# Kernel tuning notes

Hardware: AMD Instinct MI355X
Metric: run time of the kernel (lower is better)

Reference implementation:

```python
import itertools
import jax, jax.numpy as jnp
import numpy as np

NDIMS = 3
SPATIAL = (160, 160, 160)


def affine_to_dense_shift(matrix, shape, shift_center=True):
    # matrix: [ndims, ndims+1] -> displacement field [*shape, ndims]
    dt = matrix.dtype
    grids = jnp.meshgrid(*[jnp.arange(s, dtype=dt) for s in shape], indexing='ij')
    mesh = jnp.stack(grids, axis=-1)  # [D,H,W,3]
    if shift_center:
        mesh = mesh - (jnp.asarray(shape, dt) - 1.0) / 2.0
    ones = jnp.ones(mesh.shape[:-1] + (1,), dt)
    homog = jnp.concatenate([mesh, ones], axis=-1)  # [D,H,W,4]
    loc = jnp.einsum('dhwj,ij->dhwi', homog, matrix)  # [D,H,W,3]
    return loc - mesh  # displacement, invariant to the center shift


def interpn_linear(vol, loc):
    # vol: [D,H,W,C], loc: [D,H,W,3] absolute voxel coords. fill_value=None -> clip.
    D, H, W = vol.shape[:NDIMS]
    max_loc = jnp.asarray([D - 1, H - 1, W - 1], loc.dtype)
    loc = jnp.clip(loc, 0.0, max_loc)
    loc0 = jnp.clip(jnp.floor(loc), 0.0, max_loc)
    loc1 = jnp.clip(loc0 + 1.0, 0.0, max_loc)
    w_lo = loc1 - loc          # weight of the lower corner (voxelmorph convention)
    w_hi = 1.0 - w_lo          # weight of the upper corner
    loc0i = loc0.astype(jnp.int32)
    loc1i = loc1.astype(jnp.int32)
    vol_flat = vol.reshape(-1, vol.shape[-1])  # [D*H*W, C]
    out = jnp.zeros(loc.shape[:-1] + (vol.shape[-1],), vol.dtype)
    for corner in itertools.product([0, 1], repeat=NDIMS):  # 8 trilinear corners
        ii = (loc1i if corner[0] else loc0i)[..., 0]
        jj = (loc1i if corner[1] else loc0i)[..., 1]
        kk = (loc1i if corner[2] else loc0i)[..., 2]
        flat = (ii * H + jj) * W + kk
        vals = jnp.take(vol_flat, flat.reshape(-1), axis=0).reshape(out.shape)
        wt = jnp.ones(loc.shape[:-1], loc.dtype)
        for d, b in enumerate(corner):
            wt = wt * (w_hi[..., d] if b else w_lo[..., d])
        out = out + vals * wt[..., None]
    return out


def _single_transform(vol_b, aff_b):
    shift = affine_to_dense_shift(aff_b, SPATIAL, shift_center=True)  # [D,H,W,3]
    grids = jnp.meshgrid(*[jnp.arange(s, dtype=shift.dtype) for s in SPATIAL], indexing='ij')
    grid = jnp.stack(grids, axis=-1)
    return interpn_linear(vol_b, grid + shift)


def setup_inputs() -> dict:
    key = jax.random.key(0)
    k1, k2 = jax.random.split(key)
    vol = jax.random.normal(k1, (4, *SPATIAL, 2), dtype=jnp.float32)
    # near-identity affine so most sampled coordinates stay in-bounds
    eye = jnp.broadcast_to(jnp.eye(NDIMS, NDIMS + 1, dtype=jnp.float32), (4, NDIMS, NDIMS + 1))
    trf = eye + 0.1 * jax.random.normal(k2, (4, NDIMS, NDIMS + 1), dtype=jnp.float32)
    return {"vol": vol, "trf": trf}


def reference(vol, trf):
    return jax.vmap(_single_transform)(vol, trf)
```

## Files before the change

### kernel.cpp

```cpp
#include <hip/hip_runtime.h>


constexpr int D = 160, H = 160, W = 160, C = 2;
constexpr unsigned VOX_PER_B = D * H * W;
constexpr int TI = 4, TJ = 8, TK = 32;
constexpr unsigned NTI = D / TI;
constexpr unsigned NTJ = H / TJ;
constexpr unsigned NTK = W / TK;
constexpr unsigned TPV = NTI * NTJ * NTK;
constexpr unsigned NBLOCKS = 4u * TPV;
constexpr unsigned NXCD = 8;
constexpr unsigned CHUNK = NBLOCKS / NXCD;

struct VPair { float2 lo, hi; };

struct Gset { int p00, p01, p10, p11; float wxl, wyl, wzl; };

__device__ __forceinline__ Gset mkset(float lx, float ly, float lz)
{
    const float mx = 159.0f;
    lx = fminf(fmaxf(lx, 0.0f), mx);
    ly = fminf(fmaxf(ly, 0.0f), mx);
    lz = fminf(fmaxf(lz, 0.0f), mx);

    float fx0 = floorf(lx), fy0 = floorf(ly), fz0 = floorf(lz);
    float fx1 = fminf(fx0 + 1.0f, mx);
    float fy1 = fminf(fy0 + 1.0f, mx);
    float fz1 = fminf(fz0 + 1.0f, mx);

    int ix0 = (int)fx0, iy0 = (int)fy0, iz0 = (int)fz0;
    int ix1 = (int)fx1, iy1 = (int)fy1;

    Gset g;
    g.wxl = fx1 - lx; g.wyl = fy1 - ly; g.wzl = fz1 - lz;

    int zb = min(iz0, W - 2);
    int r0 = ix0 * H, r1 = ix1 * H;
    g.p00 = (r0 + iy0) * W + zb;
    g.p01 = (r0 + iy1) * W + zb;
    g.p10 = (r1 + iy0) * W + zb;
    g.p11 = (r1 + iy1) * W + zb;
    return g;
}

__device__ __forceinline__ float2 interp(VPair q00, VPair q01, VPair q10, VPair q11,
                                         const Gset& g)
{
    float wzl = g.wzl, wzh = 1.0f - wzl;
    float wyl = g.wyl, wyh = 1.0f - wyl;
    float wxl = g.wxl, wxh = 1.0f - wxl;

    float zx00 = q00.lo.x * wzl + q00.hi.x * wzh, zy00 = q00.lo.y * wzl + q00.hi.y * wzh;
    float zx01 = q01.lo.x * wzl + q01.hi.x * wzh, zy01 = q01.lo.y * wzl + q01.hi.y * wzh;
    float zx10 = q10.lo.x * wzl + q10.hi.x * wzh, zy10 = q10.lo.y * wzl + q10.hi.y * wzh;
    float zx11 = q11.lo.x * wzl + q11.hi.x * wzh, zy11 = q11.lo.y * wzl + q11.hi.y * wzh;

    float yx0 = zx00 * wyl + zx01 * wyh, yy0 = zy00 * wyl + zy01 * wyh;
    float yx1 = zx10 * wyl + zx11 * wyh, yy1 = zy10 * wyl + zy11 * wyh;

    float2 o;
    o.x = yx0 * wxl + yx1 * wxh;
    o.y = yy0 * wxl + yy1 * wxh;
    return o;
}

__global__ __launch_bounds__(256) void st_affine_trilinear(
    const float* __restrict__ vol,
    const float* __restrict__ trf,
    float* __restrict__ out)
{
    unsigned bid = blockIdx.x;
    unsigned swz = (bid & (NXCD - 1)) * CHUNK + (bid >> 3);

    unsigned b  = swz / TPV;
    unsigned r  = swz - b * TPV;
    unsigned it = r / (NTJ * NTK);
    unsigned r2 = r - it * (NTJ * NTK);
    unsigned jt = r2 / NTK;
    unsigned kt = r2 - jt * NTK;
    unsigned i0 = it * TI, j0 = jt * TJ, k0 = kt * TK;

    unsigned jl = threadIdx.x >> 5, kl = threadIdx.x & 31u;
    unsigned j = j0 + jl, k = k0 + kl;

    const float* m = trf + b * 12u;
    float m00 = m[0], m01 = m[1], m02 = m[2],  m03 = m[3];
    float m10 = m[4], m11 = m[5], m12 = m[6],  m13 = m[7];
    float m20 = m[8], m21 = m[9], m22 = m[10], m23 = m[11];

    const float cc = 79.5f;
    float xc = (float)i0 - cc, yc = (float)j - cc, zc = (float)k - cc;

    float lx = fmaf(m00, xc, fmaf(m01, yc, fmaf(m02, zc, m03 + cc)));
    float ly = fmaf(m10, xc, fmaf(m11, yc, fmaf(m12, zc, m13 + cc)));
    float lz = fmaf(m20, xc, fmaf(m21, yc, fmaf(m22, zc, m23 + cc)));

    const float2* vb = (const float2*)(vol) + (size_t)b * VOX_PER_B;
    unsigned o_idx = ((b * D + i0) * H + j) * W + k;

    Gset g0 = mkset(lx, ly, lz);
    VPair q00 = *(const VPair*)(vb + g0.p00);
    VPair q01 = *(const VPair*)(vb + g0.p01);
    VPair q10 = *(const VPair*)(vb + g0.p10);
    VPair q11 = *(const VPair*)(vb + g0.p11);

    #pragma unroll
    for (int t = 0; t < TI; ++t) {
        Gset gn;
        VPair n00, n01, n10, n11;
        if (t < TI - 1) {
            lx += m00; ly += m10; lz += m20;
            gn = mkset(lx, ly, lz);
            n00 = *(const VPair*)(vb + gn.p00);
            n01 = *(const VPair*)(vb + gn.p01);
            n10 = *(const VPair*)(vb + gn.p10);
            n11 = *(const VPair*)(vb + gn.p11);
        }

        float2 o = interp(q00, q01, q10, q11, g0);
        double od;
        __builtin_memcpy(&od, &o, 8);
        __builtin_nontemporal_store(od, (double*)out + o_idx + (unsigned)t * (H * W));

        g0 = gn; q00 = n00; q01 = n01; q10 = n10; q11 = n11;
    }
}

extern "C" void kernel_launch(void* const* d_in, const int* in_sizes, int n_in,
                              void* d_out, int out_size, void* d_ws, size_t ws_size,
                              hipStream_t stream) {
    const float* vol = (const float*)d_in[0];
    const float* trf = (const float*)d_in[1];
    float* out = (float*)d_out;

    st_affine_trilinear<<<NBLOCKS, 256, 0, stream>>>(vol, trf, out);
}
```

Measured before the change: 52.34 us.

## Double TI per thread and deepen gather prefetch to two steps

Each thread now processes eight i-slices instead of four, which halves the number of blocks and amortizes per-thread affine setup. The gather pipeline is deepened from one-ahead to two-ahead, so two sets of corner loads are in flight while the current voxel is interpolated, to hide memory latency. In exchange register pressure rises and occupancy may drop, and the smaller grid reduces parallel slack across the chip.

```diff
diff --git a/kernel.cpp b/kernel.cpp
--- a/kernel.cpp
+++ b/kernel.cpp
@@ -3,7 +3,7 @@
 
 constexpr int D = 160, H = 160, W = 160, C = 2;
 constexpr unsigned VOX_PER_B = D * H * W;
-constexpr int TI = 4, TJ = 8, TK = 32;
+constexpr int TI = 8, TJ = 8, TK = 32;
 constexpr unsigned NTI = D / TI;
 constexpr unsigned NTJ = H / TJ;
 constexpr unsigned NTK = W / TK;
@@ -98,31 +98,39 @@
     const float2* vb = (const float2*)(vol) + (size_t)b * VOX_PER_B;
     unsigned o_idx = ((b * D + i0) * H + j) * W + k;
 
-    Gset g0 = mkset(lx, ly, lz);
-    VPair q00 = *(const VPair*)(vb + g0.p00);
-    VPair q01 = *(const VPair*)(vb + g0.p01);
-    VPair q10 = *(const VPair*)(vb + g0.p10);
-    VPair q11 = *(const VPair*)(vb + g0.p11);
+    Gset gA = mkset(lx, ly, lz);
+    VPair a00 = *(const VPair*)(vb + gA.p00);
+    VPair a01 = *(const VPair*)(vb + gA.p01);
+    VPair a10 = *(const VPair*)(vb + gA.p10);
+    VPair a11 = *(const VPair*)(vb + gA.p11);
+
+    lx += m00; ly += m10; lz += m20;
+    Gset gB = mkset(lx, ly, lz);
+    VPair b00 = *(const VPair*)(vb + gB.p00);
+    VPair b01 = *(const VPair*)(vb + gB.p01);
+    VPair b10 = *(const VPair*)(vb + gB.p10);
+    VPair b11 = *(const VPair*)(vb + gB.p11);
 
     #pragma unroll
     for (int t = 0; t < TI; ++t) {
-        Gset gn;
+        Gset gN;
         VPair n00, n01, n10, n11;
-        if (t < TI - 1) {
+        if (t + 2 < TI) {
             lx += m00; ly += m10; lz += m20;
-            gn = mkset(lx, ly, lz);
-            n00 = *(const VPair*)(vb + gn.p00);
-            n01 = *(const VPair*)(vb + gn.p01);
-            n10 = *(const VPair*)(vb + gn.p10);
-            n11 = *(const VPair*)(vb + gn.p11);
+            gN = mkset(lx, ly, lz);
+            n00 = *(const VPair*)(vb + gN.p00);
+            n01 = *(const VPair*)(vb + gN.p01);
+            n10 = *(const VPair*)(vb + gN.p10);
+            n11 = *(const VPair*)(vb + gN.p11);
         }
 
-        float2 o = interp(q00, q01, q10, q11, g0);
+        float2 o = interp(a00, a01, a10, a11, gA);
         double od;
         __builtin_memcpy(&od, &o, 8);
         __builtin_nontemporal_store(od, (double*)out + o_idx + (unsigned)t * (H * W));
 
-        g0 = gn; q00 = n00; q01 = n01; q10 = n10; q11 = n11;
+        gA = gB; a00 = b00; a01 = b01; a10 = b10; a11 = b11;
+        gB = gN; b00 = n00; b01 = n01; b10 = n10; b11 = n11;
     }
 }
 
```

Measured after the change: 51.67 us. No clear change (-1.3%).
